# Optimization experiments

Measured on AMD Instinct MI355X. Metric: run time of the kernel, lower is better.

## Reference

```python
import jax, jax.numpy as jnp
import numpy as np

B, L, E, H = 32, 512, 1024, 1024


def setup_inputs() -> dict:
    key = jax.random.key(0)
    ks = jax.random.split(key, 12)
    s = 0.02
    return {
        "x": jax.random.normal(ks[0], (B, L, E), jnp.float32),
        "h0": jax.random.normal(ks[1], (B, L, H), jnp.float32),
        "c0": jax.random.normal(ks[2], (B, L, H), jnp.float32),
        "W_ioux": jax.random.normal(ks[3], (E, 3 * H), jnp.float32) * s,
        "W_iouh": jax.random.normal(ks[4], (2, H, 3 * H), jnp.float32) * s,
        "b_iouh": jax.random.normal(ks[5], (2, 3 * H), jnp.float32) * s,
        "W_fx": jax.random.normal(ks[6], (E, H), jnp.float32) * s,
        "W_fh": jax.random.normal(ks[7], (4, H, H), jnp.float32) * s,
        "b_fh": jax.random.normal(ks[8], (4, H), jnp.float32) * s,
        "tree_ids_d": jax.random.randint(ks[9], (B, L), 0, L, jnp.int32),
        "tree_ids_dr": jax.random.randint(ks[10], (B, L), 0, L, jnp.int32),
        "tree_ids_dl": jax.random.randint(ks[11], (B, L), 0, L, jnp.int32),
    }


def _scatter_add_rows(src, idx):
    # out[b, idx[b,l], :] += src[b, l, :]   (torch scatter_add_ on dim=1 with row-repeated index)
    b = jnp.arange(src.shape[0])[:, None]
    return jnp.zeros_like(src).at[b, idx].add(src)


def _gather_rows(src, idx):
    # out[b, l, :] = src[b, idx[b,l], :]    (torch gather on dim=1 with row-repeated index)
    return jnp.take_along_axis(src, idx[:, :, None], axis=1)


def _masked_scatter(dest, mask3, src):
    # torch masked_scatter_: True positions (flat order) filled with src elements in flat order
    mflat = mask3.reshape(-1)
    pos = jnp.cumsum(mflat.astype(jnp.int32)) - 1
    filled = jnp.take(src.reshape(-1), jnp.clip(pos, 0, src.size - 1))
    return jnp.where(mflat, filled, dest.reshape(-1)).reshape(dest.shape)


def reference(x, h0, c0, W_ioux, W_iouh, b_iouh, W_fx, W_fh, b_fh,
              tree_ids_d, tree_ids_dr, tree_ids_dl):
    Hh = h0.shape[-1]
    iou_x = x @ W_ioux                               # [B,L,3H]
    iou_hr = h0 @ W_iouh[0] + b_iouh[0]              # [B,L,3H]
    iou_hl = h0 @ W_iouh[1] + b_iouh[1]
    # original repeats index only to hidden_size -> only first H cols (i-gate) get scattered child states
    add = (_scatter_add_rows(iou_hr[..., :Hh], tree_ids_dr)
           + _scatter_add_rows(iou_hl[..., :Hh], tree_ids_dl))
    iou = iou_x.at[..., :Hh].add(add)
    i, o, u = jnp.split(iou, 3, axis=-1)
    i, o, u = jax.nn.sigmoid(i), jax.nn.sigmoid(o), jnp.tanh(u)

    fx = x @ W_fx                                    # [B,L,H]
    # fh[0],fh[1] both gathered at index_r; fh[2],fh[3] both at index_l -> fuse the GEMMs
    fr = h0 @ (W_fh[0] + W_fh[1]) + (b_fh[0] + b_fh[1])
    fl = h0 @ (W_fh[2] + W_fh[3]) + (b_fh[2] + b_fh[3])
    f = jax.nn.sigmoid(_gather_rows(fx, tree_ids_d)
                       + _gather_rows(fr, tree_ids_dr)
                       + _gather_rows(fl, tree_ids_dl))

    fc = f * c0
    c_new = i * u + _scatter_add_rows(fc, tree_ids_d)
    h_new = o * jnp.tanh(c_new)

    mask3 = jnp.broadcast_to((tree_ids_d != 0)[:, :, None], h_new.shape)
    h_out = _masked_scatter(h0, mask3, h_new)
    c_out = _masked_scatter(c0, mask3, c_new)
    return (h_out, c_out)
```

## Files before the change

kernel.cpp:

```cpp
#include <hip/hip_runtime.h>


#define ROWS 16384
#define HID  1024
#define KDIM 1024
#define NCOLS 4096
#define BM 256
#define BN 256

typedef __attribute__((ext_vector_type(4))) int            i32x4;
typedef __attribute__((ext_vector_type(4))) float          f32x4;
typedef __attribute__((ext_vector_type(4))) unsigned short u16x4;
typedef __attribute__((ext_vector_type(8))) unsigned short u16x8;

__device__ __forceinline__ unsigned short f2bf(float f) {
  unsigned u = __float_as_uint(f);
  unsigned r = 0x7FFFu + ((u >> 16) & 1u);
  return (unsigned short)((u + r) >> 16);
}
__device__ __forceinline__ float bf2f(unsigned short v) {
  return __uint_as_float(((unsigned)v) << 16);
}
__device__ __forceinline__ float sigmoidf_(float x) {
  return 1.0f / (1.0f + __expf(-x));
}
__device__ __forceinline__ void gload16(const void* g, void* l) {
  __builtin_amdgcn_global_load_lds(
      (const __attribute__((address_space(1))) void*)g,
      (__attribute__((address_space(3))) void*)l, 16, 0, 0);
}
__device__ __forceinline__ void mfma_bf16(f32x4& acc, i32x4 a, i32x4 b) {
  asm volatile("v_mfma_f32_16x16x32_bf16 %0, %1, %2, %0"
               : "+v"(acc) : "v"(a), "v"(b));
}


__global__ void pack_wx(const float* __restrict__ Wioux, const float* __restrict__ Wfx,
                        unsigned short* __restrict__ Wxt) {
  __shared__ float t[32][33];
  const int n0 = blockIdx.x * 32, k0 = blockIdx.y * 32;
  const int tx = threadIdx.x, ty = threadIdx.y;
  const int n = n0 + tx, k = k0 + ty;
  float v = (n < 3072) ? Wioux[(size_t)k * 3072 + n]
                       : Wfx[(size_t)k * 1024 + (n - 3072)];
  t[ty][tx] = v;
  __syncthreads();
  Wxt[(size_t)(n0 + ty) * KDIM + (k0 + tx)] = f2bf(t[tx][ty]);
}

__global__ void pack_wh(const float* __restrict__ Wiouh, const float* __restrict__ Wfh,
                        unsigned short* __restrict__ Wht) {
  __shared__ float t[32][33];
  const int n0 = blockIdx.x * 32, k0 = blockIdx.y * 32;
  const int tx = threadIdx.x, ty = threadIdx.y;
  const int n = n0 + tx, k = k0 + ty;
  float v;
  if (n < 1024)      v = Wiouh[(size_t)k * 3072 + n];
  else if (n < 2048) v = Wiouh[3145728u + (size_t)k * 3072 + (n - 1024)];
  else if (n < 3072) { const int c = n - 2048;
    v = Wfh[(size_t)k * 1024 + c] + Wfh[1048576u + (size_t)k * 1024 + c]; }
  else { const int c = n - 3072;
    v = Wfh[2097152u + (size_t)k * 1024 + c] + Wfh[3145728u + (size_t)k * 1024 + c]; }
  t[ty][tx] = v;
  __syncthreads();
  Wht[(size_t)(n0 + ty) * KDIM + (k0 + tx)] = f2bf(t[tx][ty]);
}

__global__ void pack_bias(const float* __restrict__ b_iouh, const float* __restrict__ b_fh,
                          float* __restrict__ bh) {
  const int n = blockIdx.x * 1024 + threadIdx.x;
  float v;
  if (n < 1024)      v = b_iouh[n];
  else if (n < 2048) v = b_iouh[3072 + (n - 1024)];
  else if (n < 3072) { const int c = n - 2048; v = b_fh[c] + b_fh[1024 + c]; }
  else { const int c = n - 3072; v = b_fh[2048 + c] + b_fh[3072 + c]; }
  bh[n] = v;
}

__global__ void convert_bf16(const float* __restrict__ x, const float* __restrict__ h0,
                             unsigned short* __restrict__ xb, unsigned short* __restrict__ hb) {
  const size_t i = ((size_t)blockIdx.x * 256 + threadIdx.x) * 4;
  const float4 a = *(const float4*)&x[i];
  const float4 b = *(const float4*)&h0[i];
  u16x4 av = { f2bf(a.x), f2bf(a.y), f2bf(a.z), f2bf(a.w) };
  u16x4 bv = { f2bf(b.x), f2bf(b.y), f2bf(b.z), f2bf(b.w) };
  *(u16x4*)&xb[i] = av;
  *(u16x4*)&hb[i] = bv;
}

__device__ __forceinline__ void stageR(const unsigned short* __restrict__ gp,
                                       unsigned short* __restrict__ slot,
                                       int rb, int gbase, int k0, int tid) {
  const int r = rb + (tid >> 2);
  const int sseg = (tid & 3) ^ (r & 3);
  unsigned short* lp = slot + (size_t)(rb + ((tid >> 6) << 4)) * 32;
  gload16(gp + (size_t)(gbase + r) * KDIM + k0 + sseg * 8, lp);
}

#define RD_A(qm)                                                               \
  _Pragma("unroll")                                                            \
  for (int i = 0; i < 4; ++i) {                                                \
    const int R = wr * 128 + (qm) * 64 + i * 16 + m0;                          \
    af[i] = *(const i32x4*)(Ab + R * 32 + ((kg ^ sw) << 3));                   \
  }

#define RD_B                                                                   \
  _Pragma("unroll")                                                            \
  for (int j = 0; j < 4; ++j) {                                                \
    const int Cc = wc * 64 + j * 16 + m0;                                      \
    bfr[j] = *(const i32x4*)(Bb + Cc * 32 + ((kg ^ sw) << 3));                 \
  }

#define MM(qmb)                                                                \
  __builtin_amdgcn_s_setprio(1);                                               \
  _Pragma("unroll")                                                            \
  for (int i = 0; i < 4; ++i)                                                  \
    _Pragma("unroll")                                                          \
    for (int j = 0; j < 4; ++j)                                                \
      mfma_bf16(acc[(qmb) + i][j], af[i], bfr[j]);                             \
  __builtin_amdgcn_s_setprio(0);

__global__ __launch_bounds__(512, 2)
void gemm8(const unsigned short* __restrict__ xb, const unsigned short* __restrict__ hb,
           const unsigned short* __restrict__ Wxt, const unsigned short* __restrict__ Wht,
           unsigned short* __restrict__ gxb, unsigned short* __restrict__ ghb,
           const float* __restrict__ bhv) {
  __shared__ __align__(16) unsigned short S[4][2][256][32];

  const unsigned short* A;
  const unsigned short* Bt;
  unsigned short* Cp;
  const float* bias;
  if (blockIdx.z == 0) { A = xb; Bt = Wxt; Cp = gxb; bias = nullptr; }
  else                 { A = hb; Bt = Wht; Cp = ghb; bias = bhv; }

  int bx = blockIdx.x, by = blockIdx.y;
  const int ny = gridDim.y;
  if ((ny & 7) == 0) {
    const int n = blockIdx.x + 16 * blockIdx.y;
    const int xcd = n & 7, idx = n >> 3;
    const int ych = ny >> 3;
    bx = idx / ych;
    by = xcd * ych + (idx % ych);
  }
  const int bm = by * BM, bn = bx * BN;

  const int tid = threadIdx.x, w = tid >> 6, lane = tid & 63;
  const int wr = w >> 2, wc = w & 3;
  const int m0 = lane & 15, kg = lane >> 4, sw = m0 & 3;

  f32x4 acc[8][4] = {};

  for (int tt = 0; tt < 3; ++tt) {
    stageR(A,  &S[tt][0][0][0], 0,   bm, tt * 32, tid);
    stageR(A,  &S[tt][0][0][0], 128, bm, tt * 32, tid);
    stageR(Bt, &S[tt][1][0][0], 0,   bn, tt * 32, tid);
    stageR(Bt, &S[tt][1][0][0], 128, bn, tt * 32, tid);
  }
  asm volatile("s_waitcnt vmcnt(8)" ::: "memory");
  __builtin_amdgcn_s_barrier();
  __builtin_amdgcn_sched_barrier(0);

  for (int t = 0; t < 32; ++t) {
    const int sl = t & 3;
    const unsigned short* Ab = &S[sl][0][0][0];
    const unsigned short* Bb = &S[sl][1][0][0];
    const bool st = (t < 29);
    const int sl3 = (t + 3) & 3;
    const int k3 = (t + 3) << 5;
    i32x4 af[4], bfr[4];

    RD_A(0)
    RD_B
    if (st) { stageR(A,  &S[sl3][0][0][0], 0, bm, k3, tid);
              stageR(Bt, &S[sl3][1][0][0], 0, bn, k3, tid); }
    MM(0)

    RD_A(1)
    if (st) { stageR(A,  &S[sl3][0][0][0], 128, bm, k3, tid);
              stageR(Bt, &S[sl3][1][0][0], 128, bn, k3, tid); }
    MM(4)

    if (t <= 28)      asm volatile("s_waitcnt vmcnt(8)" ::: "memory");
    else if (t == 29) asm volatile("s_waitcnt vmcnt(4)" ::: "memory");
    else if (t == 30) asm volatile("s_waitcnt vmcnt(0)" ::: "memory");
    if (t < 31) {
      __builtin_amdgcn_s_barrier();
      __builtin_amdgcn_sched_barrier(0);
    }
  }

  __builtin_amdgcn_s_barrier();
  __builtin_amdgcn_sched_barrier(0);
  unsigned short* E = &S[0][0][0][0];
  const int rg = kg * 4;
#pragma unroll
  for (int mi = 0; mi < 8; ++mi) {
#pragma unroll
    for (int nj = 0; nj < 4; ++nj) {
      const int col = wc * 64 + nj * 16 + m0;
      const float bv = bias ? bias[bn + col] : 0.0f;
      const int rowb = wr * 128 + mi * 16 + rg;
#pragma unroll
      for (int r = 0; r < 4; ++r) {
        const int row = rowb + r;
        E[row * 256 + (col ^ (((row >> 2) & 3) << 4))] = f2bf(acc[mi][nj][r] + bv);
      }
    }
  }
  __syncthreads();
#pragma unroll
  for (int jj = 0; jj < 16; ++jj) {
    const int row = jj * 16 + (tid >> 5);
    const int c0 = (tid & 31) * 8;
    const int cs = c0 ^ (((row >> 2) & 3) << 4);
    const u16x8 v = *(const u16x8*)&E[row * 256 + cs];
    *(u16x8*)&Cp[(size_t)(bm + row) * NCOLS + bn + c0] = v;
  }
}

__global__ void scan_mask(const int* __restrict__ idd, int* __restrict__ sel,
                          int* __restrict__ mcount) {
  __shared__ int ps[1024];
  const int t = threadIdx.x;
  int loc[16];
  int cnt = 0;
#pragma unroll
  for (int i = 0; i < 16; ++i) {
    const int v = (idd[t * 16 + i] != 0) ? 1 : 0;
    loc[i] = v; cnt += v;
  }
  ps[t] = cnt;
  __syncthreads();
  for (int off = 1; off < 1024; off <<= 1) {
    const int add = (t >= off) ? ps[t - off] : 0;
    __syncthreads();
    ps[t] += add;
    __syncthreads();
  }
  int rank = (t == 0) ? 0 : ps[t - 1];
#pragma unroll
  for (int i = 0; i < 16; ++i)
    if (loc[i]) sel[rank++] = t * 16 + i;
  if (t == 1023) *mcount = ps[1023];
}

__global__ void build_csr(const int* __restrict__ idd, const int* __restrict__ idr,
                          const int* __restrict__ idl,
                          int* __restrict__ ofsD, int* __restrict__ ofsR, int* __restrict__ ofsL,
                          int* __restrict__ lstD, int* __restrict__ lstR, int* __restrict__ lstL) {
  __shared__ int sidx[512];
  __shared__ int scan[512];
  const int b = blockIdx.x, t = threadIdx.x;
  const int gb = b << 9;
  const int* const srcs[3] = { idd, idr, idl };
  int* const ofss[3] = { ofsD, ofsR, ofsL };
  int* const lsts[3] = { lstD, lstR, lstL };
  for (int a = 0; a < 3; ++a) {
    sidx[t] = srcs[a][gb + t];
    scan[t] = 0;
    __syncthreads();
    atomicAdd(&scan[sidx[t]], 1);
    __syncthreads();
    int v = scan[t];
    for (int off = 1; off < 512; off <<= 1) {
      const int add = (t >= off) ? scan[t - off] : 0;
      __syncthreads();
      scan[t] += add;
      __syncthreads();
    }
    const int start = scan[t] - v;
    ofss[a][b * 513 + t] = start;
    if (t == 511) ofss[a][b * 513 + 512] = scan[511];
    int pos = start;
    for (int l = 0; l < 512; ++l)
      if (sidx[l] == t) lsts[a][gb + (pos++)] = l;
    __syncthreads();
  }
}

__global__ __launch_bounds__(256)
void fused_final(const unsigned short* __restrict__ gxb, const unsigned short* __restrict__ ghb,
                 const float* __restrict__ h0, const float* __restrict__ c0,
                 const int* __restrict__ idd, const int* __restrict__ idr,
                 const int* __restrict__ idl,
                 const int* __restrict__ ofsR, const int* __restrict__ lstR,
                 const int* __restrict__ ofsL, const int* __restrict__ lstL,
                 const int* __restrict__ ofsD, const int* __restrict__ lstD,
                 const int* __restrict__ sel, const int* __restrict__ mcount,
                 float* __restrict__ hout, float* __restrict__ cout, int r0) {
  const int r = blockIdx.x;
  const int g = r0 + r;
  const int j = g & 511;
  const int bb = g >> 9;
  const int lbase = (r >> 9) << 9;
  const int ob = bb * 513;
  const int lb = bb << 9;
  const int c = threadIdx.x << 2;

  float a0 = 0.f, a1 = 0.f, a2 = 0.f, a3 = 0.f;
  for (int q = ofsR[ob + j], e = ofsR[ob + j + 1]; q < e; ++q) {
    const int l = lstR[lb + q];
    const u16x4 v = *(const u16x4*)&ghb[(size_t)(lbase + l) * NCOLS + c];
    a0 += bf2f(v[0]); a1 += bf2f(v[1]); a2 += bf2f(v[2]); a3 += bf2f(v[3]);
  }
  for (int q = ofsL[ob + j], e = ofsL[ob + j + 1]; q < e; ++q) {
    const int l = lstL[lb + q];
    const u16x4 v = *(const u16x4*)&ghb[(size_t)(lbase + l) * NCOLS + 1024 + c];
    a0 += bf2f(v[0]); a1 += bf2f(v[1]); a2 += bf2f(v[2]); a3 += bf2f(v[3]);
  }

  const u16x4 fx4 = *(const u16x4*)&gxb[(size_t)r * NCOLS + 3072 + c];
  const float fx0 = bf2f(fx4[0]), fx1 = bf2f(fx4[1]), fx2 = bf2f(fx4[2]), fx3 = bf2f(fx4[3]);
  float fc0 = 0.f, fc1 = 0.f, fc2 = 0.f, fc3 = 0.f;
  for (int q = ofsD[ob + j], e = ofsD[ob + j + 1]; q < e; ++q) {
    const int l = lstD[lb + q];
    const int jr = idr[lb + l], jl = idl[lb + l];
    const u16x4 rv = *(const u16x4*)&ghb[(size_t)(lbase + jr) * NCOLS + 2048 + c];
    const u16x4 lv = *(const u16x4*)&ghb[(size_t)(lbase + jl) * NCOLS + 3072 + c];
    const float4 cc = *(const float4*)&c0[(size_t)(lb + l) * HID + c];
    fc0 += sigmoidf_(fx0 + bf2f(rv[0]) + bf2f(lv[0])) * cc.x;
    fc1 += sigmoidf_(fx1 + bf2f(rv[1]) + bf2f(lv[1])) * cc.y;
    fc2 += sigmoidf_(fx2 + bf2f(rv[2]) + bf2f(lv[2])) * cc.z;
    fc3 += sigmoidf_(fx3 + bf2f(rv[3]) + bf2f(lv[3])) * cc.w;
  }

  const u16x4 vi = *(const u16x4*)&gxb[(size_t)r * NCOLS + c];
  const u16x4 vo = *(const u16x4*)&gxb[(size_t)r * NCOLS + 1024 + c];
  const u16x4 vu = *(const u16x4*)&gxb[(size_t)r * NCOLS + 2048 + c];
  float4 hn, cn;
  {
    const float ig = sigmoidf_(bf2f(vi[0]) + a0), og = sigmoidf_(bf2f(vo[0]));
    cn.x = ig * tanhf(bf2f(vu[0])) + fc0; hn.x = og * tanhf(cn.x);
  }
  {
    const float ig = sigmoidf_(bf2f(vi[1]) + a1), og = sigmoidf_(bf2f(vo[1]));
    cn.y = ig * tanhf(bf2f(vu[1])) + fc1; hn.y = og * tanhf(cn.y);
  }
  {
    const float ig = sigmoidf_(bf2f(vi[2]) + a2), og = sigmoidf_(bf2f(vo[2]));
    cn.z = ig * tanhf(bf2f(vu[2])) + fc2; hn.z = og * tanhf(cn.z);
  }
  {
    const float ig = sigmoidf_(bf2f(vi[3]) + a3), og = sigmoidf_(bf2f(vo[3]));
    cn.w = ig * tanhf(bf2f(vu[3])) + fc3; hn.w = og * tanhf(cn.w);
  }

  if (idd[g] == 0) {
    *(float4*)&hout[(size_t)g * HID + c] = *(const float4*)&h0[(size_t)g * HID + c];
    *(float4*)&cout[(size_t)g * HID + c] = *(const float4*)&c0[(size_t)g * HID + c];
  }
  const int m = *mcount;
  if (g < m) {
    const int o = sel[g];
    *(float4*)&hout[(size_t)o * HID + c] = hn;
    *(float4*)&cout[(size_t)o * HID + c] = cn;
  }
}

extern "C" void kernel_launch(void* const* d_in, const int* in_sizes, int n_in,
                              void* d_out, int out_size, void* d_ws, size_t ws_size,
                              hipStream_t stream) {
  const float* x      = (const float*)d_in[0];
  const float* h0     = (const float*)d_in[1];
  const float* c0     = (const float*)d_in[2];
  const float* W_ioux = (const float*)d_in[3];
  const float* W_iouh = (const float*)d_in[4];
  const float* b_iouh = (const float*)d_in[5];
  const float* W_fx   = (const float*)d_in[6];
  const float* W_fh   = (const float*)d_in[7];
  const float* b_fh   = (const float*)d_in[8];
  const int* idd      = (const int*)d_in[9];
  const int* idr      = (const int*)d_in[10];
  const int* idl      = (const int*)d_in[11];
  float* hout = (float*)d_out;
  float* cout = hout + (size_t)ROWS * HID;

  char* ws = (char*)d_ws;
  unsigned short* Wxt  = (unsigned short*)(ws);
  unsigned short* Wht  = (unsigned short*)(ws + 8388608u);
  float*          bh   = (float*)(ws + 16777216u);
  int*            sel  = (int*)(ws + 16793600u);
  int*            mcnt = (int*)(ws + 16859136u);
  int*            ofsD = (int*)(ws + 16859392u);
  int*            ofsR = (int*)(ws + 16925184u);
  int*            ofsL = (int*)(ws + 16990976u);
  int*            lstD = (int*)(ws + 17056768u);
  int*            lstR = (int*)(ws + 17122304u);
  int*            lstL = (int*)(ws + 17187840u);
  const size_t    base = 17253376u;

  int C = 32;
  while (C > 1 && base + 10485760ull * (size_t)C > ws_size) C >>= 1;
  const int R = 512 * C;

  char* p = ws + base;
  unsigned short* xb  = (unsigned short*)p;  p += 1048576ull * C;
  unsigned short* hb  = (unsigned short*)p;  p += 1048576ull * C;
  unsigned short* gxb = (unsigned short*)p;  p += 4194304ull * C;
  unsigned short* ghb = (unsigned short*)p;

  pack_wx<<<dim3(128, 32), dim3(32, 32), 0, stream>>>(W_ioux, W_fx, Wxt);
  pack_wh<<<dim3(128, 32), dim3(32, 32), 0, stream>>>(W_iouh, W_fh, Wht);
  pack_bias<<<4, 1024, 0, stream>>>(b_iouh, b_fh, bh);
  scan_mask<<<1, 1024, 0, stream>>>(idd, sel, mcnt);
  build_csr<<<32, 512, 0, stream>>>(idd, idr, idl, ofsD, ofsR, ofsL, lstD, lstR, lstL);

  for (int b0 = 0; b0 < 32; b0 += C) {
    const size_t r0 = (size_t)b0 * 512;
    convert_bf16<<<R, 256, 0, stream>>>(x + r0 * HID, h0 + r0 * HID, xb, hb);
    gemm8<<<dim3(NCOLS / BN, R / BM, 2), 512, 0, stream>>>(xb, hb, Wxt, Wht, gxb, ghb, bh);
    fused_final<<<R, 256, 0, stream>>>(gxb, ghb, h0, c0, idd, idr, idl,
                                       ofsR, lstR, ofsL, lstL, ofsD, lstD,
                                       sel, mcnt, hout, cout, (int)r0);
  }
}
```

Baseline: 547.0 us.

## Shrink GEMM tile to 128x256 with 3-stage LDS pipeline for higher occupancy

Replaces the 256x256-tile, 4-stage GEMM with a 128x256 tile and a 3-slot LDS ring buffer. It cuts accumulators from 32 to 16 per wave and raises launch bounds to 4 blocks per CU. It also changes the LDS swizzle pattern and how the prefetch distance is scheduled. The aim is more concurrent blocks to hide latency, at the cost of lower arithmetic intensity per tile and more total A/B traffic.

```diff
diff --git a/kernel.cpp b/kernel.cpp
--- a/kernel.cpp
+++ b/kernel.cpp
@@ -5,8 +5,9 @@
 #define HID  1024
 #define KDIM 1024
 #define NCOLS 4096
-#define BM 256
+#define BM 128
 #define BN 256
+#define SLOT 12288
 
 typedef __attribute__((ext_vector_type(4))) int            i32x4;
 typedef __attribute__((ext_vector_type(4))) float          f32x4;
@@ -88,44 +89,27 @@
   *(u16x4*)&hb[i] = bv;
 }
 
-__device__ __forceinline__ void stageR(const unsigned short* __restrict__ gp,
-                                       unsigned short* __restrict__ slot,
-                                       int rb, int gbase, int k0, int tid) {
-  const int r = rb + (tid >> 2);
-  const int sseg = (tid & 3) ^ (r & 3);
-  unsigned short* lp = slot + (size_t)(rb + ((tid >> 6) << 4)) * 32;
-  gload16(gp + (size_t)(gbase + r) * KDIM + k0 + sseg * 8, lp);
-}
-
-#define RD_A(qm)                                                               \
-  _Pragma("unroll")                                                            \
-  for (int i = 0; i < 4; ++i) {                                                \
-    const int R = wr * 128 + (qm) * 64 + i * 16 + m0;                          \
-    af[i] = *(const i32x4*)(Ab + R * 32 + ((kg ^ sw) << 3));                   \
-  }
-
-#define RD_B                                                                   \
-  _Pragma("unroll")                                                            \
-  for (int j = 0; j < 4; ++j) {                                                \
-    const int Cc = wc * 64 + j * 16 + m0;                                      \
-    bfr[j] = *(const i32x4*)(Bb + Cc * 32 + ((kg ^ sw) << 3));                 \
-  }
-
-#define MM(qmb)                                                                \
-  __builtin_amdgcn_s_setprio(1);                                               \
-  _Pragma("unroll")                                                            \
-  for (int i = 0; i < 4; ++i)                                                  \
-    _Pragma("unroll")                                                          \
-    for (int j = 0; j < 4; ++j)                                                \
-      mfma_bf16(acc[(qmb) + i][j], af[i], bfr[j]);                             \
-  __builtin_amdgcn_s_setprio(0);
-
-__global__ __launch_bounds__(512, 2)
-void gemm8(const unsigned short* __restrict__ xb, const unsigned short* __restrict__ hb,
-           const unsigned short* __restrict__ Wxt, const unsigned short* __restrict__ Wht,
-           unsigned short* __restrict__ gxb, unsigned short* __restrict__ ghb,
-           const float* __restrict__ bhv) {
-  __shared__ __align__(16) unsigned short S[4][2][256][32];
+__device__ __forceinline__ void stageA(const unsigned short* __restrict__ gp,
+                                       unsigned short* __restrict__ slotA,
+                                       int bm, int k0, int tid, int w) {
+  const int r = tid >> 2;
+  const int sseg = (tid & 3) ^ ((r >> 1) & 3);
+  gload16(gp + (size_t)(bm + r) * KDIM + k0 + sseg * 8, slotA + w * 512);
+}
+__device__ __forceinline__ void stageB(const unsigned short* __restrict__ gp,
+                                       unsigned short* __restrict__ slotB,
+                                       int bn, int k0, int tid, int w, int q) {
+  const int r = (q << 7) + (tid >> 2);
+  const int sseg = (tid & 3) ^ ((r >> 1) & 3);
+  gload16(gp + (size_t)(bn + r) * KDIM + k0 + sseg * 8, slotB + q * 4096 + w * 512);
+}
+
+__global__ __launch_bounds__(512, 4)
+void gemm3s(const unsigned short* __restrict__ xb, const unsigned short* __restrict__ hb,
+            const unsigned short* __restrict__ Wxt, const unsigned short* __restrict__ Wht,
+            unsigned short* __restrict__ gxb, unsigned short* __restrict__ ghb,
+            const float* __restrict__ bhv) {
+  __shared__ __align__(16) unsigned short Sm[3 * SLOT];
 
   const unsigned short* A;
   const unsigned short* Bt;
@@ -147,60 +131,68 @@
 
   const int tid = threadIdx.x, w = tid >> 6, lane = tid & 63;
   const int wr = w >> 2, wc = w & 3;
-  const int m0 = lane & 15, kg = lane >> 4, sw = m0 & 3;
-
-  f32x4 acc[8][4] = {};
-
-  for (int tt = 0; tt < 3; ++tt) {
-    stageR(A,  &S[tt][0][0][0], 0,   bm, tt * 32, tid);
-    stageR(A,  &S[tt][0][0][0], 128, bm, tt * 32, tid);
-    stageR(Bt, &S[tt][1][0][0], 0,   bn, tt * 32, tid);
-    stageR(Bt, &S[tt][1][0][0], 128, bn, tt * 32, tid);
-  }
-  asm volatile("s_waitcnt vmcnt(8)" ::: "memory");
+  const int m0 = lane & 15, kg = lane >> 4;
+  const int sw = (m0 >> 1) & 3;
+  const int koff = (kg ^ sw) << 3;
+
+  f32x4 acc[4][4] = {};
+
+  stageA(A,  Sm,                bm, 0,  tid, w);
+  stageB(Bt, Sm + 4096,         bn, 0,  tid, w, 0);
+  stageB(Bt, Sm + 4096,         bn, 0,  tid, w, 1);
+  stageA(A,  Sm + SLOT,         bm, 32, tid, w);
+  stageB(Bt, Sm + SLOT + 4096,  bn, 32, tid, w, 0);
+  stageB(Bt, Sm + SLOT + 4096,  bn, 32, tid, w, 1);
+  asm volatile("s_waitcnt vmcnt(3)" ::: "memory");
   __builtin_amdgcn_s_barrier();
   __builtin_amdgcn_sched_barrier(0);
 
+  int cur = 0;
   for (int t = 0; t < 32; ++t) {
-    const int sl = t & 3;
-    const unsigned short* Ab = &S[sl][0][0][0];
-    const unsigned short* Bb = &S[sl][1][0][0];
-    const bool st = (t < 29);
-    const int sl3 = (t + 3) & 3;
-    const int k3 = (t + 3) << 5;
+    unsigned short* Ab = Sm + cur * SLOT;
+    unsigned short* Bb = Ab + 4096;
+    if (t < 30) {
+      const int n2 = (cur + 2 >= 3) ? cur - 1 : cur + 2;
+      unsigned short* An = Sm + n2 * SLOT;
+      const int k2 = (t + 2) << 5;
+      stageA(A,  An,        bm, k2, tid, w);
+      stageB(Bt, An + 4096, bn, k2, tid, w, 0);
+      stageB(Bt, An + 4096, bn, k2, tid, w, 1);
+    }
     i32x4 af[4], bfr[4];
-
-    RD_A(0)
-    RD_B
-    if (st) { stageR(A,  &S[sl3][0][0][0], 0, bm, k3, tid);
-              stageR(Bt, &S[sl3][1][0][0], 0, bn, k3, tid); }
-    MM(0)
-
-    RD_A(1)
-    if (st) { stageR(A,  &S[sl3][0][0][0], 128, bm, k3, tid);
-              stageR(Bt, &S[sl3][1][0][0], 128, bn, k3, tid); }
-    MM(4)
-
-    if (t <= 28)      asm volatile("s_waitcnt vmcnt(8)" ::: "memory");
-    else if (t == 29) asm volatile("s_waitcnt vmcnt(4)" ::: "memory");
+#pragma unroll
+    for (int i = 0; i < 4; ++i)
+      af[i] = *(const i32x4*)(Ab + (wr * 64 + i * 16 + m0) * 32 + koff);
+#pragma unroll
+    for (int j = 0; j < 4; ++j)
+      bfr[j] = *(const i32x4*)(Bb + (wc * 64 + j * 16 + m0) * 32 + koff);
+    __builtin_amdgcn_s_setprio(1);
+#pragma unroll
+    for (int i = 0; i < 4; ++i)
+#pragma unroll
+      for (int j = 0; j < 4; ++j)
+        mfma_bf16(acc[i][j], af[i], bfr[j]);
+    __builtin_amdgcn_s_setprio(0);
+    if (t < 30)       asm volatile("s_waitcnt vmcnt(3)" ::: "memory");
     else if (t == 30) asm volatile("s_waitcnt vmcnt(0)" ::: "memory");
     if (t < 31) {
       __builtin_amdgcn_s_barrier();
       __builtin_amdgcn_sched_barrier(0);
     }
+    cur = (cur + 1 == 3) ? 0 : cur + 1;
   }
 
   __builtin_amdgcn_s_barrier();
   __builtin_amdgcn_sched_barrier(0);
-  unsigned short* E = &S[0][0][0][0];
+  unsigned short* E = Sm;
   const int rg = kg * 4;
 #pragma unroll
-  for (int mi = 0; mi < 8; ++mi) {
+  for (int mi = 0; mi < 4; ++mi) {
 #pragma unroll
     for (int nj = 0; nj < 4; ++nj) {
       const int col = wc * 64 + nj * 16 + m0;
       const float bv = bias ? bias[bn + col] : 0.0f;
-      const int rowb = wr * 128 + mi * 16 + rg;
+      const int rowb = wr * 64 + mi * 16 + rg;
 #pragma unroll
       for (int r = 0; r < 4; ++r) {
         const int row = rowb + r;
@@ -210,7 +202,7 @@
   }
   __syncthreads();
 #pragma unroll
-  for (int jj = 0; jj < 16; ++jj) {
+  for (int jj = 0; jj < 8; ++jj) {
     const int row = jj * 16 + (tid >> 5);
     const int c0 = (tid & 31) * 8;
     const int cs = c0 ^ (((row >> 2) & 3) << 4);
@@ -409,7 +401,7 @@
   for (int b0 = 0; b0 < 32; b0 += C) {
     const size_t r0 = (size_t)b0 * 512;
     convert_bf16<<<R, 256, 0, stream>>>(x + r0 * HID, h0 + r0 * HID, xb, hb);
-    gemm8<<<dim3(NCOLS / BN, R / BM, 2), 512, 0, stream>>>(xb, hb, Wxt, Wht, gxb, ghb, bh);
+    gemm3s<<<dim3(NCOLS / BN, R / BM, 2), 512, 0, stream>>>(xb, hb, Wxt, Wht, gxb, ghb, bh);
     fused_final<<<R, 256, 0, stream>>>(gxb, ghb, h0, c0, idd, idr, idl,
                                        ofsR, lstR, ofsL, lstL, ofsD, lstD,
                                        sel, mcnt, hout, cout, (int)r0);
```

New measurement: 525.9 us. 1.04x faster.

## Double-buffer LDS fragments in registers across K-steps of the bf16 GEMM

Applied to the files above, without the earlier changes.

Restructures the gemm8 main loop so the A/B fragments for the next K-slice are read from shared memory into a second register set while MFMAs run on the current set. The loop is unrolled by two, and the wait and barrier logic is retuned so two stages are resident before compute starts. The LDS swizzle changes to XOR on (row>>1)&3, applied consistently to the stores and the reads, to change the bank-conflict pattern. Launch bounds drop to one block per CU to make room for the larger register footprint, which trades occupancy for latency hiding. The XCD block remap is now applied unconditionally.

```diff
diff --git a/kernel.cpp b/kernel.cpp
--- a/kernel.cpp
+++ b/kernel.cpp
@@ -92,35 +92,12 @@
                                        unsigned short* __restrict__ slot,
                                        int rb, int gbase, int k0, int tid) {
   const int r = rb + (tid >> 2);
-  const int sseg = (tid & 3) ^ (r & 3);
+  const int sseg = (tid & 3) ^ ((r >> 1) & 3);
   unsigned short* lp = slot + (size_t)(rb + ((tid >> 6) << 4)) * 32;
   gload16(gp + (size_t)(gbase + r) * KDIM + k0 + sseg * 8, lp);
 }
 
-#define RD_A(qm)                                                               \
-  _Pragma("unroll")                                                            \
-  for (int i = 0; i < 4; ++i) {                                                \
-    const int R = wr * 128 + (qm) * 64 + i * 16 + m0;                          \
-    af[i] = *(const i32x4*)(Ab + R * 32 + ((kg ^ sw) << 3));                   \
-  }
-
-#define RD_B                                                                   \
-  _Pragma("unroll")                                                            \
-  for (int j = 0; j < 4; ++j) {                                                \
-    const int Cc = wc * 64 + j * 16 + m0;                                      \
-    bfr[j] = *(const i32x4*)(Bb + Cc * 32 + ((kg ^ sw) << 3));                 \
-  }
-
-#define MM(qmb)                                                                \
-  __builtin_amdgcn_s_setprio(1);                                               \
-  _Pragma("unroll")                                                            \
-  for (int i = 0; i < 4; ++i)                                                  \
-    _Pragma("unroll")                                                          \
-    for (int j = 0; j < 4; ++j)                                                \
-      mfma_bf16(acc[(qmb) + i][j], af[i], bfr[j]);                             \
-  __builtin_amdgcn_s_setprio(0);
-
-__global__ __launch_bounds__(512, 2)
+__global__ __launch_bounds__(512, 1)
 void gemm8(const unsigned short* __restrict__ xb, const unsigned short* __restrict__ hb,
            const unsigned short* __restrict__ Wxt, const unsigned short* __restrict__ Wht,
            unsigned short* __restrict__ gxb, unsigned short* __restrict__ ghb,
@@ -135,11 +112,10 @@
   else                 { A = hb; Bt = Wht; Cp = ghb; bias = bhv; }
 
   int bx = blockIdx.x, by = blockIdx.y;
-  const int ny = gridDim.y;
-  if ((ny & 7) == 0) {
+  {
     const int n = blockIdx.x + 16 * blockIdx.y;
     const int xcd = n & 7, idx = n >> 3;
-    const int ych = ny >> 3;
+    const int ych = gridDim.y >> 3;
     bx = idx / ych;
     by = xcd * ych + (idx % ych);
   }
@@ -147,44 +123,62 @@
 
   const int tid = threadIdx.x, w = tid >> 6, lane = tid & 63;
   const int wr = w >> 2, wc = w & 3;
-  const int m0 = lane & 15, kg = lane >> 4, sw = m0 & 3;
+  const int m0 = lane & 15, kg = lane >> 4;
+  const int koff = (kg ^ ((m0 >> 1) & 3)) << 3;
 
   f32x4 acc[8][4] = {};
-
-  for (int tt = 0; tt < 3; ++tt) {
-    stageR(A,  &S[tt][0][0][0], 0,   bm, tt * 32, tid);
-    stageR(A,  &S[tt][0][0][0], 128, bm, tt * 32, tid);
-    stageR(Bt, &S[tt][1][0][0], 0,   bn, tt * 32, tid);
-    stageR(Bt, &S[tt][1][0][0], 128, bn, tt * 32, tid);
-  }
-  asm volatile("s_waitcnt vmcnt(8)" ::: "memory");
+  i32x4 afX[8], bfX[4], afY[8], bfY[4];
+
+#define READF(AF, BF, SL)                                                      \
+  {                                                                            \
+    const unsigned short* Ab = &S[SL][0][0][0];                                \
+    const unsigned short* Bb = &S[SL][1][0][0];                                \
+    _Pragma("unroll")                                                          \
+    for (int i = 0; i < 8; ++i)                                                \
+      AF[i] = *(const i32x4*)(Ab + (wr * 128 + i * 16 + m0) * 32 + koff);      \
+    _Pragma("unroll")                                                          \
+    for (int j = 0; j < 4; ++j)                                                \
+      BF[j] = *(const i32x4*)(Bb + (wc * 64 + j * 16 + m0) * 32 + koff);       \
+  }
+
+#define MMF(AF, BF)                                                            \
+  __builtin_amdgcn_s_setprio(1);                                               \
+  _Pragma("unroll")                                                            \
+  for (int i = 0; i < 8; ++i)                                                  \
+    _Pragma("unroll")                                                          \
+    for (int j = 0; j < 4; ++j)                                                \
+      mfma_bf16(acc[i][j], AF[i], BF[j]);                                      \
+  __builtin_amdgcn_s_setprio(0);
+
+#define STAGE(T)                                                               \
+  { const int kk = (T) << 5; const int sl = (T) & 3;                           \
+    stageR(A,  &S[sl][0][0][0], 0,   bm, kk, tid);                             \
+    stageR(A,  &S[sl][0][0][0], 128, bm, kk, tid);                             \
+    stageR(Bt, &S[sl][1][0][0], 0,   bn, kk, tid);                             \
+    stageR(Bt, &S[sl][1][0][0], 128, bn, kk, tid); }
+
+  STAGE(0) STAGE(1) STAGE(2)
+  asm volatile("s_waitcnt vmcnt(4)" ::: "memory");
   __builtin_amdgcn_s_barrier();
   __builtin_amdgcn_sched_barrier(0);
-
-  for (int t = 0; t < 32; ++t) {
-    const int sl = t & 3;
-    const unsigned short* Ab = &S[sl][0][0][0];
-    const unsigned short* Bb = &S[sl][1][0][0];
-    const bool st = (t < 29);
-    const int sl3 = (t + 3) & 3;
-    const int k3 = (t + 3) << 5;
-    i32x4 af[4], bfr[4];
-
-    RD_A(0)
-    RD_B
-    if (st) { stageR(A,  &S[sl3][0][0][0], 0, bm, k3, tid);
-              stageR(Bt, &S[sl3][1][0][0], 0, bn, k3, tid); }
-    MM(0)
-
-    RD_A(1)
-    if (st) { stageR(A,  &S[sl3][0][0][0], 128, bm, k3, tid);
-              stageR(Bt, &S[sl3][1][0][0], 128, bn, k3, tid); }
-    MM(4)
-
-    if (t <= 28)      asm volatile("s_waitcnt vmcnt(8)" ::: "memory");
-    else if (t == 29) asm volatile("s_waitcnt vmcnt(4)" ::: "memory");
-    else if (t == 30) asm volatile("s_waitcnt vmcnt(0)" ::: "memory");
-    if (t < 31) {
+  READF(afX, bfX, 0)
+
+#pragma unroll 1
+  for (int tt = 0; tt < 16; ++tt) {
+    const int t0 = tt * 2;
+    if (t0 <= 28) STAGE(t0 + 3)
+    READF(afY, bfY, (t0 + 1) & 3)
+    MMF(afX, bfX)
+    if (t0 <= 28)      asm volatile("s_waitcnt vmcnt(4)" ::: "memory");
+    __builtin_amdgcn_s_barrier();
+    __builtin_amdgcn_sched_barrier(0);
+    const int t1 = t0 + 1;
+    if (t1 <= 28) STAGE(t1 + 3)
+    if (t1 < 31) READF(afX, bfX, (t1 + 1) & 3)
+    MMF(afY, bfY)
+    if (t1 <= 28)      asm volatile("s_waitcnt vmcnt(4)" ::: "memory");
+    else if (t1 == 29) asm volatile("s_waitcnt vmcnt(0)" ::: "memory");
+    if (t1 < 31) {
       __builtin_amdgcn_s_barrier();
       __builtin_amdgcn_sched_barrier(0);
     }
@@ -217,6 +211,9 @@
     const u16x8 v = *(const u16x8*)&E[row * 256 + cs];
     *(u16x8*)&Cp[(size_t)(bm + row) * NCOLS + bn + c0] = v;
   }
+#undef READF
+#undef MMF
+#undef STAGE
 }
 
 __global__ void scan_mask(const int* __restrict__ idd, int* __restrict__ sel,
```

New measurement: 541.8 us. About the same (-1.0%).
